# Optimization experiments

Measured on AMD Instinct MI355X. Metric: run time of the kernel, lower is better.

## Reference

```python
import jax, jax.numpy as jnp
import numpy as np

BIG = 1e6  # sentinel 'no zero pixel found yet' distance; BIG**2 = 1e12 fits fp32


def _edt(is_fg):
    """Exact Euclidean distance transform (scipy.distance_transform_edt semantics):
    distance from each nonzero pixel to the nearest zero pixel. is_fg: [N,H,W] bool.
    Separable exact algorithm: 1D vertical distance-to-zero per column via cummax
    scans, then min-plus convolution with the parabola (j-k)^2 along rows."""
    N, H, W = is_fg.shape
    is_zero = ~is_fg
    ih = jnp.arange(H, dtype=jnp.float32)[None, :, None]
    # nearest zero at-or-above / at-or-below along H (per column)
    up = jax.lax.cummax(jnp.where(is_zero, ih, -BIG), axis=1)
    dn = -jax.lax.cummax(jnp.where(is_zero, -ih, -BIG), axis=1, reverse=True)
    g = jnp.minimum(ih - up, dn - ih)               # [N,H,W] vertical 1D distance
    g2 = jnp.minimum(g, BIG) ** 2
    ks = jnp.arange(W, dtype=jnp.float32)
    def col(j):
        # exact 2D squared distance for output column j: min_k (j-k)^2 + g(.,.,k)^2
        return jnp.min((j.astype(jnp.float32) - ks) ** 2 + g2, axis=-1)  # [N,H]
    d2 = jax.lax.map(col, jnp.arange(W))            # [W,N,H], sequential -> low memory
    return jnp.sqrt(jnp.moveaxis(d2, 0, -1))        # [N,H,W]


def setup_inputs() -> dict:
    key = jax.random.key(0)
    k1, k2 = jax.random.split(key)
    B, C, H, W = 8, 12, 256, 256
    logits = jax.random.normal(k1, (B, C, H, W), dtype=jnp.float32)
    targets = jax.random.randint(k2, (B, H, W), 0, C, dtype=jnp.int32)
    return {"logits": logits, "targets": targets}


def reference(logits, targets):
    B, C, H, W = logits.shape
    probs = jax.nn.softmax(logits, axis=1)                                  # [B,C,H,W]
    gt = targets[:, None, :, :] == jnp.arange(C, dtype=targets.dtype)[None, :, None, None]
    m = gt.reshape(B * C, H, W)
    pos = _edt(m)          # distance inside foreground to nearest background
    neg = _edt(~m)         # distance inside background to nearest foreground
    dt = (neg - pos).reshape(B, C, H, W)
    has_fg = gt.any(axis=(2, 3))                                            # [B,C]
    dt = jnp.where(has_fg[:, :, None, None], dt, 0.0)
    # per-image, per-class min-max normalization (matches torch view(B,-1).min/max)
    dmin = dt.min(axis=(2, 3), keepdims=True)
    dmax = dt.max(axis=(2, 3), keepdims=True)
    dt = (dt - dmin) / (dmax - dmin + 1e-8)
    inter = jnp.sum(probs * dt, axis=(2, 3))                                # [B,C]
    denom = jnp.sum(probs * probs, axis=(2, 3)) + jnp.sum(dt * dt, axis=(2, 3)) + 1e-6
    dice = 2.0 * inter / denom
    # sum_c mean_b (1-dice) / C  == mean over (b,c) since ignore_index=255 is out of range
    return jnp.mean(1.0 - dice)
```

## Files before the change

### kernel.cpp

```cpp
#include <hip/hip_runtime.h>
#include <math.h>

constexpr int B_  = 8;
constexpr int C_  = 12;
constexpr int H_  = 256;
constexpr int W_  = 256;
constexpr int HW_ = H_ * W_;
constexpr int NBC_ = B_ * C_;
constexpr int SUMX_ = 32;
constexpr int PAD_ = 256;


__global__ void k_vert(const int* __restrict__ t,
                       unsigned short* __restrict__ gpk,
                       int* __restrict__ hasfg_p) {
    constexpr int SEG = 8, SH = 32;
    int tid = threadIdx.x;
    int s  = tid >> 5;
    int wl = tid & 31;
    int blk = blockIdx.x;
    int bc = blk >> 3;
    int w0 = (blk & 7) * 32;
    int b = bc / C_, c = bc - b * C_;
    int w = w0 + wl;
    const int* base = t + b * HW_ + w;
    int h0 = s * SH;

    unsigned tp[SH / 4];
    int lastEq = -1, lastNeq = -1, firstEq = 256, firstNeq = 256;
    #pragma unroll 8
    for (int i = 0; i < SH; ++i) {
        int tv = base[(h0 + i) * W_];
        if ((i & 3) == 0) tp[i >> 2] = 0;
        tp[i >> 2] |= (unsigned)tv << ((i & 3) * 8);
        int h = h0 + i;
        if (tv == c) { lastEq = h;  if (firstEq  == 256) firstEq  = h; }
        else         { lastNeq = h; if (firstNeq == 256) firstNeq = h; }
    }
    __shared__ int sLE[SEG][32], sLN[SEG][32], sFE[SEG][32], sFN[SEG][32];
    sLE[s][wl] = lastEq; sLN[s][wl] = lastNeq;
    sFE[s][wl] = firstEq; sFN[s][wl] = firstNeq;
    __syncthreads();

    int carLE = -1, carLN = -1;
    for (int q = 0; q < s; ++q) {
        carLE = max(carLE, sLE[q][wl]);
        carLN = max(carLN, sLN[q][wl]);
    }
    int carFE = 256, carFN = 256;
    for (int q = s + 1; q < SEG; ++q) {
        carFE = min(carFE, sFE[q][wl]);
        carFN = min(carFN, sFN[q][wl]);
    }
    bool pred = (s == SEG - 1) && (max(carLE, lastEq) >= 0);
    bool anyfg = __any(pred);
    if (tid == 192) hasfg_p[blk] = anyfg ? 1 : 0;

    int pLE[SH], pLN[SH];
    {
        int le = carLE, ln = carLN;
        #pragma unroll
        for (int i = 0; i < SH; ++i) {
            int tv = (tp[i >> 2] >> ((i & 3) * 8)) & 0xFF;
            int h = h0 + i;
            if (tv == c) le = h; else ln = h;
            pLE[i] = le; pLN[i] = ln;
        }
    }
    {
        int fe = carFE, fn = carFN;
        unsigned short* gk = gpk + (size_t)bc * HW_ + w;
        #pragma unroll
        for (int i = SH - 1; i >= 0; --i) {
            int tv = (tp[i >> 2] >> ((i & 3) * 8)) & 0xFF;
            int h = h0 + i;
            if (tv == c) fe = h; else fn = h;
            bool fg = (tv == c);
            int lastZ = fg ? pLN[i] : pLE[i];
            int nextZ = fg ? fn : fe;
            int dl = (lastZ < 0)   ? 0x7FFF : (h - lastZ);
            int dnx = (nextZ > 255) ? 0x7FFF : (nextZ - h);
            int d = min(dl, dnx);
            gk[h * W_] = (unsigned short)(d | (fg ? 0x8000 : 0));
        }
    }
}

__global__ void k_horiz(const unsigned short* __restrict__ gpk,
                        const int* __restrict__ hasfg_p, float* __restrict__ dt,
                        float* __restrict__ pmn, float* __restrict__ pmx) {
    __shared__ float sp[4][W_ + 2 * PAD_];
    __shared__ float sn[4][W_ + 2 * PAD_];
    __shared__ float bmn[4], bmx[4];
    int wave = threadIdx.x >> 6;
    int lane = threadIdx.x & 63;
    int row = blockIdx.x * 4 + wave;
    int bc = row >> 8;
    float* drow = dt + (size_t)row * W_;

    int hfl = 0;
    if (lane < 8) hfl = hasfg_p[bc * 8 + lane];
    bool hf = __any(hfl != 0);

    if (!hf) {
        #pragma unroll
        for (int i = 0; i < 4; ++i) drow[lane + 64 * i] = 0.0f;
        if (threadIdx.x == 0) { pmn[blockIdx.x] = 0.0f; pmx[blockIdx.x] = 0.0f; }
        return;
    }

    float4 inf4 = make_float4(3.0e38f, 3.0e38f, 3.0e38f, 3.0e38f);
    ((float4*)&sp[wave][0])[lane]          = inf4;
    ((float4*)&sp[wave][PAD_ + W_])[lane]  = inf4;
    ((float4*)&sn[wave][0])[lane]          = inf4;
    ((float4*)&sn[wave][PAD_ + W_])[lane]  = inf4;

    int hh = row & (H_ - 1);
    float s1 = (float)(1000000 - hh);
    float sent2 = s1 * s1;
    const ushort4 v4 = ((const ushort4*)(gpk + (size_t)row * W_))[lane];
    float4 fpv, fnv;
    {
        const unsigned short* vs = (const unsigned short*)&v4;
        float* fp = (float*)&fpv;
        float* fn = (float*)&fnv;
        #pragma unroll
        for (int q = 0; q < 4; ++q) {
            unsigned v = vs[q];
            unsigned d = v & 0x7FFFu;
            float g2 = (d == 0x7FFFu) ? sent2 : (float)(d * d);
            bool fg = (v & 0x8000u) != 0;
            fp[q] = fg ? g2 : 0.0f;
            fn[q] = fg ? 0.0f : g2;
        }
    }
    ((float4*)&sp[wave][PAD_])[lane] = fpv;
    ((float4*)&sn[wave][PAD_])[lane] = fnv;
    __syncthreads();

    float bp[4], bn[4];
    #pragma unroll
    for (int i = 0; i < 4; ++i) {
        int j = PAD_ + lane + 64 * i;
        bp[i] = sp[wave][j];
        bn[i] = sn[wave][j];
    }
    for (int r = 1; r < W_; ++r) {
        float fr = (float)r;
        float r2 = fr * fr;
        float m = fmaxf(fmaxf(bn[0], bn[1]), fmaxf(bn[2], bn[3]));
        if (!__any(r2 < m)) break;
        #pragma unroll
        for (int i = 0; i < 4; ++i) {
            int j = PAD_ + lane + 64 * i;
            float v = fminf(sn[wave][j - r], sn[wave][j + r]);
            bn[i] = fminf(bn[i], fmaf(fr, fr, v));
        }
    }
    for (int r = 1; r < W_; ++r) {
        float fr = (float)r;
        float r2 = fr * fr;
        float m = fmaxf(fmaxf(bp[0], bp[1]), fmaxf(bp[2], bp[3]));
        if (!__any(r2 < m)) break;
        #pragma unroll
        for (int i = 0; i < 4; ++i) {
            int j = PAD_ + lane + 64 * i;
            float v = fminf(sp[wave][j - r], sp[wave][j + r]);
            bp[i] = fminf(bp[i], fmaf(fr, fr, v));
        }
    }

    float dval[4], mn = 3.4e38f, mx = -3.4e38f;
    #pragma unroll
    for (int i = 0; i < 4; ++i) {
        dval[i] = sqrtf(bn[i]) - sqrtf(bp[i]);
        mn = fminf(mn, dval[i]);
        mx = fmaxf(mx, dval[i]);
    }
    #pragma unroll
    for (int off = 32; off; off >>= 1) {
        mn = fminf(mn, __shfl_xor(mn, off));
        mx = fmaxf(mx, __shfl_xor(mx, off));
    }
    if (lane == 0) { bmn[wave] = mn; bmx[wave] = mx; }
    __syncthreads();
    if (threadIdx.x == 0) {
        pmn[blockIdx.x] = fminf(fminf(bmn[0], bmn[1]), fminf(bmn[2], bmn[3]));
        pmx[blockIdx.x] = fmaxf(fmaxf(bmx[0], bmx[1]), fmaxf(bmx[2], bmx[3]));
    }
    #pragma unroll
    for (int i = 0; i < 4; ++i) drow[lane + 64 * i] = dval[i];
}

__global__ void k_sums(const float* __restrict__ logits, const float* __restrict__ dt,
                       const float* __restrict__ pmn, const float* __restrict__ pmx,
                       float* __restrict__ accum_p) {
    int b = blockIdx.y;
    int tid = threadIdx.x;
    __shared__ float snorm[C_ * 2];
    __shared__ float sI[4][C_], sP[4][C_], sD[4][C_];

    if (tid < C_ * 16) {
        int c = tid >> 4, j = tid & 15;
        float mn = 3.4e38f, mx = -3.4e38f;
        #pragma unroll
        for (int q = 0; q < 4; ++q) {
            int idx = (b * C_ + c) * 64 + j * 4 + q;
            mn = fminf(mn, pmn[idx]);
            mx = fmaxf(mx, pmx[idx]);
        }
        #pragma unroll
        for (int off = 8; off; off >>= 1) {
            mn = fminf(mn, __shfl_xor(mn, off));
            mx = fmaxf(mx, __shfl_xor(mx, off));
        }
        if (j == 0) {
            snorm[c * 2]     = mn;
            snorm[c * 2 + 1] = 1.0f / (mx - mn + 1e-8f);
        }
    }
    __syncthreads();

    const float* lb = logits + (size_t)b * C_ * HW_;
    const float* db = dt + (size_t)b * C_ * HW_;

    float inter[C_], p2[C_], d2s[C_];
    #pragma unroll
    for (int c = 0; c < C_; ++c) { inter[c] = 0.f; p2[c] = 0.f; d2s[c] = 0.f; }

    for (int p = blockIdx.x * blockDim.x + tid; p < HW_;
         p += gridDim.x * blockDim.x) {
        float l[C_];
        float mxl = -3.4e38f;
        #pragma unroll
        for (int c = 0; c < C_; ++c) { l[c] = lb[c * HW_ + p]; mxl = fmaxf(mxl, l[c]); }
        float s = 0.f;
        #pragma unroll
        for (int c = 0; c < C_; ++c) { l[c] = expf(l[c] - mxl); s += l[c]; }
        float inv = 1.0f / s;
        #pragma unroll
        for (int c = 0; c < C_; ++c) {
            float pr = l[c] * inv;
            float dv = db[c * HW_ + p];
            float dn = (dv - snorm[c * 2]) * snorm[c * 2 + 1];
            inter[c] = fmaf(pr, dn, inter[c]);
            p2[c]    = fmaf(pr, pr, p2[c]);
            d2s[c]   = fmaf(dn, dn, d2s[c]);
        }
    }

    int lane = tid & 63;
    int wave = tid >> 6;
    #pragma unroll
    for (int c = 0; c < C_; ++c) {
        float a = inter[c], p = p2[c], d = d2s[c];
        #pragma unroll
        for (int off = 32; off; off >>= 1) {
            a += __shfl_down(a, off);
            p += __shfl_down(p, off);
            d += __shfl_down(d, off);
        }
        if (lane == 0) { sI[wave][c] = a; sP[wave][c] = p; sD[wave][c] = d; }
    }
    __syncthreads();
    if (tid < C_ * 3) {
        int c = tid % C_;
        int comp = tid / C_;
        float v = 0.f;
        #pragma unroll
        for (int w = 0; w < 4; ++w)
            v += (comp == 0) ? sI[w][c] : (comp == 1) ? sP[w][c] : sD[w][c];
        accum_p[(((size_t)b * SUMX_ + blockIdx.x) * C_ + c) * 3 + comp] = v;
    }
}

__global__ void k_final(const float* __restrict__ accum_p, float* __restrict__ out) {
    int tid = threadIdx.x;
    float v = 0.f;
    if (tid < NBC_) {
        int b = tid / C_, c = tid - b * C_;
        float inter = 0.f, p2 = 0.f, d2 = 0.f;
        for (int gx = 0; gx < SUMX_; ++gx) {
            size_t base = (((size_t)b * SUMX_ + gx) * C_ + c) * 3;
            inter += accum_p[base];
            p2    += accum_p[base + 1];
            d2    += accum_p[base + 2];
        }
        float dice = 2.0f * inter / (p2 + d2 + 1e-6f);
        v = 1.0f - dice;
    }
    #pragma unroll
    for (int off = 32; off; off >>= 1) v += __shfl_down(v, off);
    __shared__ float s2[2];
    if ((tid & 63) == 0) s2[tid >> 6] = v;
    __syncthreads();
    if (tid == 0) out[0] = (s2[0] + s2[1]) / (float)NBC_;
}

extern "C" void kernel_launch(void* const* d_in, const int* in_sizes, int n_in,
                              void* d_out, int out_size, void* d_ws, size_t ws_size,
                              hipStream_t stream) {
    const float* logits  = (const float*)d_in[0];
    const int*   targets = (const int*)d_in[1];
    float* out = (float*)d_out;

    float* dt    = (float*)d_ws;
    float* pmn   = dt + (size_t)NBC_ * HW_;
    float* pmx   = pmn + NBC_ * 64;
    float* accum = pmx + NBC_ * 64;
    unsigned short* gpk = (unsigned short*)(accum + (size_t)B_ * SUMX_ * C_ * 3);
    int* hasfg_p = (int*)(gpk + (size_t)NBC_ * HW_);

    k_vert<<<NBC_ * 8, 256, 0, stream>>>(targets, gpk, hasfg_p);
    k_horiz<<<NBC_ * H_ / 4, 256, 0, stream>>>(gpk, hasfg_p, dt, pmn, pmx);
    k_sums<<<dim3(SUMX_, B_), 256, 0, stream>>>(logits, dt, pmn, pmx, accum);
    k_final<<<1, 128, 0, stream>>>(accum, out);
}
```

Before: 120.8 us.

## Fuse softmax dice sums into EDT row kernel and expand normalization algebraically

The separate dt buffer, the k_sums pass and the final kernel are removed. Each EDT row wave now computes softmax for its class over that row and accumulates raw moments (sum p·d, p, p², d, d²) plus the row's min and max. A per-(b,c) reduction kernel then applies the min-max normalization algebraically and accumulates the loss with an atomicAdd, after a memset of the output. This avoids writing and re-reading a full float distance map. In exchange, each logits row is re-read and its softmax recomputed once per class, and the expanded sum of squares can lose precision through cancellation.

After: 133.3 us. 1.1x slower.

```diff
diff --git a/kernel.cpp b/kernel.cpp
--- a/kernel.cpp
+++ b/kernel.cpp
@@ -7,7 +7,6 @@
 constexpr int W_  = 256;
 constexpr int HW_ = H_ * W_;
 constexpr int NBC_ = B_ * C_;
-constexpr int SUMX_ = 32;
 constexpr int PAD_ = 256;
 
 
@@ -78,7 +77,7 @@
             bool fg = (tv == c);
             int lastZ = fg ? pLN[i] : pLE[i];
             int nextZ = fg ? fn : fe;
-            int dl = (lastZ < 0)   ? 0x7FFF : (h - lastZ);
+            int dl  = (lastZ < 0)   ? 0x7FFF : (h - lastZ);
             int dnx = (nextZ > 255) ? 0x7FFF : (nextZ - h);
             int d = min(dl, dnx);
             gk[h * W_] = (unsigned short)(d | (fg ? 0x8000 : 0));
@@ -86,215 +85,168 @@
     }
 }
 
-__global__ void k_horiz(const unsigned short* __restrict__ gpk,
-                        const int* __restrict__ hasfg_p, float* __restrict__ dt,
-                        float* __restrict__ pmn, float* __restrict__ pmx) {
+__global__ void k_edt(const unsigned short* __restrict__ gpk,
+                      const float* __restrict__ logits,
+                      const int* __restrict__ hasfg_p,
+                      float* __restrict__ part) {
     __shared__ float sp[4][W_ + 2 * PAD_];
     __shared__ float sn[4][W_ + 2 * PAD_];
-    __shared__ float bmn[4], bmx[4];
     int wave = threadIdx.x >> 6;
     int lane = threadIdx.x & 63;
     int row = blockIdx.x * 4 + wave;
     int bc = row >> 8;
-    float* drow = dt + (size_t)row * W_;
+    int b = bc / C_, c = bc - b * C_;
+    int h = row & (H_ - 1);
 
     int hfl = 0;
     if (lane < 8) hfl = hasfg_p[bc * 8 + lane];
     bool hf = __any(hfl != 0);
 
-    if (!hf) {
-        #pragma unroll
-        for (int i = 0; i < 4; ++i) drow[lane + 64 * i] = 0.0f;
-        if (threadIdx.x == 0) { pmn[blockIdx.x] = 0.0f; pmx[blockIdx.x] = 0.0f; }
-        return;
-    }
-
-    float4 inf4 = make_float4(3.0e38f, 3.0e38f, 3.0e38f, 3.0e38f);
-    ((float4*)&sp[wave][0])[lane]          = inf4;
-    ((float4*)&sp[wave][PAD_ + W_])[lane]  = inf4;
-    ((float4*)&sn[wave][0])[lane]          = inf4;
-    ((float4*)&sn[wave][PAD_ + W_])[lane]  = inf4;
-
-    int hh = row & (H_ - 1);
-    float s1 = (float)(1000000 - hh);
-    float sent2 = s1 * s1;
-    const ushort4 v4 = ((const ushort4*)(gpk + (size_t)row * W_))[lane];
-    float4 fpv, fnv;
-    {
-        const unsigned short* vs = (const unsigned short*)&v4;
-        float* fp = (float*)&fpv;
-        float* fn = (float*)&fnv;
-        #pragma unroll
-        for (int q = 0; q < 4; ++q) {
-            unsigned v = vs[q];
-            unsigned d = v & 0x7FFFu;
-            float g2 = (d == 0x7FFFu) ? sent2 : (float)(d * d);
-            bool fg = (v & 0x8000u) != 0;
-            fp[q] = fg ? g2 : 0.0f;
-            fn[q] = fg ? 0.0f : g2;
-        }
-    }
-    ((float4*)&sp[wave][PAD_])[lane] = fpv;
-    ((float4*)&sn[wave][PAD_])[lane] = fnv;
-    __syncthreads();
-
-    float bp[4], bn[4];
+    float dv[4];
+    if (hf) {
+        float4 inf4 = make_float4(3.0e38f, 3.0e38f, 3.0e38f, 3.0e38f);
+        ((float4*)&sp[wave][0])[lane]          = inf4;
+        ((float4*)&sp[wave][PAD_ + W_])[lane]  = inf4;
+        ((float4*)&sn[wave][0])[lane]          = inf4;
+        ((float4*)&sn[wave][PAD_ + W_])[lane]  = inf4;
+
+        float s1 = (float)(1000000 - h);
+        float sent2 = s1 * s1;
+        const ushort4 v4 = ((const ushort4*)(gpk + (size_t)row * W_))[lane];
+        float4 fpv, fnv;
+        {
+            const unsigned short* vs = (const unsigned short*)&v4;
+            float* fp = (float*)&fpv;
+            float* fn = (float*)&fnv;
+            #pragma unroll
+            for (int q = 0; q < 4; ++q) {
+                unsigned v = vs[q];
+                unsigned d = v & 0x7FFFu;
+                float g2 = (d == 0x7FFFu) ? sent2 : (float)(d * d);
+                bool fg = (v & 0x8000u) != 0;
+                fp[q] = fg ? g2 : 0.0f;
+                fn[q] = fg ? 0.0f : g2;
+            }
+        }
+        ((float4*)&sp[wave][PAD_])[lane] = fpv;
+        ((float4*)&sn[wave][PAD_])[lane] = fnv;
+        __syncthreads();
+
+        float bp[4], bn[4];
+        #pragma unroll
+        for (int i = 0; i < 4; ++i) {
+            int j = PAD_ + lane + 64 * i;
+            bp[i] = sp[wave][j];
+            bn[i] = sn[wave][j];
+        }
+        for (int r = 1; r < W_; ++r) {
+            float fr = (float)r;
+            float r2 = fr * fr;
+            float m = fmaxf(fmaxf(bn[0], bn[1]), fmaxf(bn[2], bn[3]));
+            if (!__any(r2 < m)) break;
+            #pragma unroll
+            for (int i = 0; i < 4; ++i) {
+                int j = PAD_ + lane + 64 * i;
+                float v = fminf(sn[wave][j - r], sn[wave][j + r]);
+                bn[i] = fminf(bn[i], fmaf(fr, fr, v));
+            }
+        }
+        for (int r = 1; r < W_; ++r) {
+            float fr = (float)r;
+            float r2 = fr * fr;
+            float m = fmaxf(fmaxf(bp[0], bp[1]), fmaxf(bp[2], bp[3]));
+            if (!__any(r2 < m)) break;
+            #pragma unroll
+            for (int i = 0; i < 4; ++i) {
+                int j = PAD_ + lane + 64 * i;
+                float v = fminf(sp[wave][j - r], sp[wave][j + r]);
+                bp[i] = fminf(bp[i], fmaf(fr, fr, v));
+            }
+        }
+        #pragma unroll
+        for (int i = 0; i < 4; ++i) dv[i] = sqrtf(bn[i]) - sqrtf(bp[i]);
+    } else {
+        #pragma unroll
+        for (int i = 0; i < 4; ++i) dv[i] = 0.0f;
+    }
+
+    const float* lrow = logits + (size_t)b * C_ * HW_ + h * W_;
+    float s_pd = 0.f, s_p = 0.f, s_pp = 0.f, s_d = 0.f, s_dd = 0.f;
+    float mn = 3.4e38f, mx = -3.4e38f;
     #pragma unroll
     for (int i = 0; i < 4; ++i) {
-        int j = PAD_ + lane + 64 * i;
-        bp[i] = sp[wave][j];
-        bn[i] = sn[wave][j];
-    }
-    for (int r = 1; r < W_; ++r) {
-        float fr = (float)r;
-        float r2 = fr * fr;
-        float m = fmaxf(fmaxf(bn[0], bn[1]), fmaxf(bn[2], bn[3]));
-        if (!__any(r2 < m)) break;
-        #pragma unroll
-        for (int i = 0; i < 4; ++i) {
-            int j = PAD_ + lane + 64 * i;
-            float v = fminf(sn[wave][j - r], sn[wave][j + r]);
-            bn[i] = fminf(bn[i], fmaf(fr, fr, v));
-        }
-    }
-    for (int r = 1; r < W_; ++r) {
-        float fr = (float)r;
-        float r2 = fr * fr;
-        float m = fmaxf(fmaxf(bp[0], bp[1]), fmaxf(bp[2], bp[3]));
-        if (!__any(r2 < m)) break;
-        #pragma unroll
-        for (int i = 0; i < 4; ++i) {
-            int j = PAD_ + lane + 64 * i;
-            float v = fminf(sp[wave][j - r], sp[wave][j + r]);
-            bp[i] = fminf(bp[i], fmaf(fr, fr, v));
-        }
-    }
-
-    float dval[4], mn = 3.4e38f, mx = -3.4e38f;
-    #pragma unroll
-    for (int i = 0; i < 4; ++i) {
-        dval[i] = sqrtf(bn[i]) - sqrtf(bp[i]);
-        mn = fminf(mn, dval[i]);
-        mx = fmaxf(mx, dval[i]);
+        int j = lane + 64 * i;
+        float l[C_];
+        float mxl = -3.4e38f;
+        #pragma unroll
+        for (int cc = 0; cc < C_; ++cc) { l[cc] = lrow[cc * HW_ + j]; mxl = fmaxf(mxl, l[cc]); }
+        float s = 0.f;
+        #pragma unroll
+        for (int cc = 0; cc < C_; ++cc) { l[cc] = expf(l[cc] - mxl); s += l[cc]; }
+        float pr = l[c] * (1.0f / s);
+        float d = dv[i];
+        s_pd = fmaf(pr, d, s_pd);
+        s_p += pr;
+        s_pp = fmaf(pr, pr, s_pp);
+        s_d += d;
+        s_dd = fmaf(d, d, s_dd);
+        mn = fminf(mn, d);
+        mx = fmaxf(mx, d);
     }
     #pragma unroll
     for (int off = 32; off; off >>= 1) {
-        mn = fminf(mn, __shfl_xor(mn, off));
-        mx = fmaxf(mx, __shfl_xor(mx, off));
-    }
-    if (lane == 0) { bmn[wave] = mn; bmx[wave] = mx; }
+        s_pd += __shfl_down(s_pd, off);
+        s_p  += __shfl_down(s_p, off);
+        s_pp += __shfl_down(s_pp, off);
+        s_d  += __shfl_down(s_d, off);
+        s_dd += __shfl_down(s_dd, off);
+        mn = fminf(mn, __shfl_down(mn, off));
+        mx = fmaxf(mx, __shfl_down(mx, off));
+    }
+    if (lane == 0) {
+        float* p8 = part + (size_t)row * 8;
+        p8[0] = s_pd; p8[1] = s_p; p8[2] = s_pp;
+        p8[3] = s_d;  p8[4] = s_dd; p8[5] = mn; p8[6] = mx;
+    }
+}
+
+__global__ void k_bcred(const float* __restrict__ part, float* __restrict__ out) {
+    int bc = blockIdx.x;
+    int tid = threadIdx.x;
+    const float* p8 = part + ((size_t)bc * 256 + tid) * 8;
+    float s_pd = p8[0], s_p = p8[1], s_pp = p8[2];
+    float s_d = p8[3], s_dd = p8[4], mn = p8[5], mx = p8[6];
+    #pragma unroll
+    for (int off = 32; off; off >>= 1) {
+        s_pd += __shfl_down(s_pd, off);
+        s_p  += __shfl_down(s_p, off);
+        s_pp += __shfl_down(s_pp, off);
+        s_d  += __shfl_down(s_d, off);
+        s_dd += __shfl_down(s_dd, off);
+        mn = fminf(mn, __shfl_down(mn, off));
+        mx = fmaxf(mx, __shfl_down(mx, off));
+    }
+    __shared__ float red[4][7];
+    int wave = tid >> 6, lane = tid & 63;
+    if (lane == 0) {
+        red[wave][0] = s_pd; red[wave][1] = s_p; red[wave][2] = s_pp;
+        red[wave][3] = s_d;  red[wave][4] = s_dd; red[wave][5] = mn; red[wave][6] = mx;
+    }
     __syncthreads();
-    if (threadIdx.x == 0) {
-        pmn[blockIdx.x] = fminf(fminf(bmn[0], bmn[1]), fminf(bmn[2], bmn[3]));
-        pmx[blockIdx.x] = fmaxf(fmaxf(bmx[0], bmx[1]), fmaxf(bmx[2], bmx[3]));
-    }
-    #pragma unroll
-    for (int i = 0; i < 4; ++i) drow[lane + 64 * i] = dval[i];
-}
-
-__global__ void k_sums(const float* __restrict__ logits, const float* __restrict__ dt,
-                       const float* __restrict__ pmn, const float* __restrict__ pmx,
-                       float* __restrict__ accum_p) {
-    int b = blockIdx.y;
-    int tid = threadIdx.x;
-    __shared__ float snorm[C_ * 2];
-    __shared__ float sI[4][C_], sP[4][C_], sD[4][C_];
-
-    if (tid < C_ * 16) {
-        int c = tid >> 4, j = tid & 15;
-        float mn = 3.4e38f, mx = -3.4e38f;
-        #pragma unroll
-        for (int q = 0; q < 4; ++q) {
-            int idx = (b * C_ + c) * 64 + j * 4 + q;
-            mn = fminf(mn, pmn[idx]);
-            mx = fmaxf(mx, pmx[idx]);
-        }
-        #pragma unroll
-        for (int off = 8; off; off >>= 1) {
-            mn = fminf(mn, __shfl_xor(mn, off));
-            mx = fmaxf(mx, __shfl_xor(mx, off));
-        }
-        if (j == 0) {
-            snorm[c * 2]     = mn;
-            snorm[c * 2 + 1] = 1.0f / (mx - mn + 1e-8f);
-        }
-    }
-    __syncthreads();
-
-    const float* lb = logits + (size_t)b * C_ * HW_;
-    const float* db = dt + (size_t)b * C_ * HW_;
-
-    float inter[C_], p2[C_], d2s[C_];
-    #pragma unroll
-    for (int c = 0; c < C_; ++c) { inter[c] = 0.f; p2[c] = 0.f; d2s[c] = 0.f; }
-
-    for (int p = blockIdx.x * blockDim.x + tid; p < HW_;
-         p += gridDim.x * blockDim.x) {
-        float l[C_];
-        float mxl = -3.4e38f;
-        #pragma unroll
-        for (int c = 0; c < C_; ++c) { l[c] = lb[c * HW_ + p]; mxl = fmaxf(mxl, l[c]); }
-        float s = 0.f;
-        #pragma unroll
-        for (int c = 0; c < C_; ++c) { l[c] = expf(l[c] - mxl); s += l[c]; }
-        float inv = 1.0f / s;
-        #pragma unroll
-        for (int c = 0; c < C_; ++c) {
-            float pr = l[c] * inv;
-            float dv = db[c * HW_ + p];
-            float dn = (dv - snorm[c * 2]) * snorm[c * 2 + 1];
-            inter[c] = fmaf(pr, dn, inter[c]);
-            p2[c]    = fmaf(pr, pr, p2[c]);
-            d2s[c]   = fmaf(dn, dn, d2s[c]);
-        }
-    }
-
-    int lane = tid & 63;
-    int wave = tid >> 6;
-    #pragma unroll
-    for (int c = 0; c < C_; ++c) {
-        float a = inter[c], p = p2[c], d = d2s[c];
-        #pragma unroll
-        for (int off = 32; off; off >>= 1) {
-            a += __shfl_down(a, off);
-            p += __shfl_down(p, off);
-            d += __shfl_down(d, off);
-        }
-        if (lane == 0) { sI[wave][c] = a; sP[wave][c] = p; sD[wave][c] = d; }
-    }
-    __syncthreads();
-    if (tid < C_ * 3) {
-        int c = tid % C_;
-        int comp = tid / C_;
-        float v = 0.f;
-        #pragma unroll
-        for (int w = 0; w < 4; ++w)
-            v += (comp == 0) ? sI[w][c] : (comp == 1) ? sP[w][c] : sD[w][c];
-        accum_p[(((size_t)b * SUMX_ + blockIdx.x) * C_ + c) * 3 + comp] = v;
-    }
-}
-
-__global__ void k_final(const float* __restrict__ accum_p, float* __restrict__ out) {
-    int tid = threadIdx.x;
-    float v = 0.f;
-    if (tid < NBC_) {
-        int b = tid / C_, c = tid - b * C_;
-        float inter = 0.f, p2 = 0.f, d2 = 0.f;
-        for (int gx = 0; gx < SUMX_; ++gx) {
-            size_t base = (((size_t)b * SUMX_ + gx) * C_ + c) * 3;
-            inter += accum_p[base];
-            p2    += accum_p[base + 1];
-            d2    += accum_p[base + 2];
-        }
-        float dice = 2.0f * inter / (p2 + d2 + 1e-6f);
-        v = 1.0f - dice;
-    }
-    #pragma unroll
-    for (int off = 32; off; off >>= 1) v += __shfl_down(v, off);
-    __shared__ float s2[2];
-    if ((tid & 63) == 0) s2[tid >> 6] = v;
-    __syncthreads();
-    if (tid == 0) out[0] = (s2[0] + s2[1]) / (float)NBC_;
+    if (tid == 0) {
+        s_pd = red[0][0]; s_p = red[0][1]; s_pp = red[0][2];
+        s_d = red[0][3]; s_dd = red[0][4]; mn = red[0][5]; mx = red[0][6];
+        for (int w = 1; w < 4; ++w) {
+            s_pd += red[w][0]; s_p += red[w][1]; s_pp += red[w][2];
+            s_d += red[w][3]; s_dd += red[w][4];
+            mn = fminf(mn, red[w][5]); mx = fmaxf(mx, red[w][6]);
+        }
+        float sc = 1.0f / (mx - mn + 1e-8f);
+        float inter = sc * (s_pd - mn * s_p);
+        float d2 = sc * sc * (s_dd - 2.0f * mn * s_d + mn * mn * (float)HW_);
+        float dice = 2.0f * inter / (s_pp + d2 + 1e-6f);
+        atomicAdd(out, (1.0f - dice) * (1.0f / (float)NBC_));
+    }
 }
 
 extern "C" void kernel_launch(void* const* d_in, const int* in_sizes, int n_in,
@@ -304,15 +256,12 @@
     const int*   targets = (const int*)d_in[1];
     float* out = (float*)d_out;
 
-    float* dt    = (float*)d_ws;
-    float* pmn   = dt + (size_t)NBC_ * HW_;
-    float* pmx   = pmn + NBC_ * 64;
-    float* accum = pmx + NBC_ * 64;
-    unsigned short* gpk = (unsigned short*)(accum + (size_t)B_ * SUMX_ * C_ * 3);
+    unsigned short* gpk = (unsigned short*)d_ws;
     int* hasfg_p = (int*)(gpk + (size_t)NBC_ * HW_);
-
+    float* part = (float*)(hasfg_p + NBC_ * 8);
+
+    hipMemsetAsync(out, 0, sizeof(float), stream);
     k_vert<<<NBC_ * 8, 256, 0, stream>>>(targets, gpk, hasfg_p);
-    k_horiz<<<NBC_ * H_ / 4, 256, 0, stream>>>(gpk, hasfg_p, dt, pmn, pmx);
-    k_sums<<<dim3(SUMX_, B_), 256, 0, stream>>>(logits, dt, pmn, pmx, accum);
-    k_final<<<1, 128, 0, stream>>>(accum, out);
-}
+    k_edt<<<NBC_ * H_ / 4, 256, 0, stream>>>(gpk, logits, hasfg_p, part);
+    k_bcred<<<NBC_, 256, 0, stream>>>(part, out);
+}
```
